# Kernel tuning notes

Hardware: AMD Instinct MI355X
Metric: run time of the kernel (lower is better)

## Reference

```python
import jax, jax.numpy as jnp
import numpy as np


def _maxpool2x2(x):
    # x: [N, C, H, W] -> [N, C, H//2, W//2]
    N, C, H, W = x.shape
    x = x.reshape(N, C, H // 2, 2, W // 2, 2)
    return x.max(axis=(3, 5))


def setup_inputs() -> dict:
    key = jax.random.key(0)
    ks = jax.random.split(key, 6)
    N, C, H, W = 16, 64, 64, 64
    x = jax.random.normal(ks[0], (N, C, H, W), dtype=jnp.float32)
    # 1x1 conv weights, stored as [out_ch, in_ch] (kernel is 1x1, no bias)
    w_theta = jax.random.normal(ks[1], (C >> 3, C), dtype=jnp.float32) * 0.05
    w_phi = jax.random.normal(ks[2], (C >> 3, C), dtype=jnp.float32) * 0.05
    w_g = jax.random.normal(ks[3], (C >> 1, C), dtype=jnp.float32) * 0.05
    w_o = jax.random.normal(ks[4], (C, C >> 1), dtype=jnp.float32) * 0.05
    gamma = jax.random.normal(ks[5], (), dtype=jnp.float32)
    return {"x": x, "w_theta": w_theta, "w_phi": w_phi, "w_g": w_g, "w_o": w_o, "gamma": gamma}


def reference(x, w_theta, w_phi, w_g, w_o, gamma):
    N, C, H, W = x.shape
    L = H * W           # location_num
    D = L >> 2          # downsampled_num
    # 1x1 convs as channel contractions
    theta = jnp.einsum('oc,nchw->nohw', w_theta, x).reshape(N, C >> 3, L)
    phi = _maxpool2x2(jnp.einsum('oc,nchw->nohw', w_phi, x)).reshape(N, C >> 3, D)
    attn = jax.nn.softmax(jnp.einsum('nkl,nkd->nld', theta, phi), axis=-1)  # [N, L, D]
    g = _maxpool2x2(jnp.einsum('oc,nchw->nohw', w_g, x)).reshape(N, C >> 1, D)
    attn_g = jnp.einsum('ngd,nld->ngl', g, attn).reshape(N, C >> 1, H, W)
    attn_g = jnp.einsum('og,nghw->nohw', w_o, attn_g)
    return x + gamma * attn_g
```

## Files before the change

kernel.cpp:

```cpp
#include <hip/hip_runtime.h>
#include <hip/hip_bf16.h>
#include <hip/hip_fp16.h>

#define NB 16
#define CCH 64
#define LL 4096
#define DD 1024

typedef _Float16 h8 __attribute__((ext_vector_type(8)));
typedef _Float16 h2 __attribute__((ext_vector_type(2)));
typedef float    f4v __attribute__((ext_vector_type(4)));

#if defined(__has_builtin)
#if __has_builtin(__builtin_amdgcn_fdot2)
#define HAVE_FDOT2 1
#endif
#if __has_builtin(__builtin_amdgcn_exp2f)
#define EXP2F(x) __builtin_amdgcn_exp2f(x)
#endif
#endif
#ifndef EXP2F
#define EXP2F(x) exp2f(x)
#endif

static __device__ __forceinline__ float fdot2f(h2 a, h2 b, float c) {
#ifdef HAVE_FDOT2
    return __builtin_amdgcn_fdot2(a, b, c, false);
#else
    return c + (float)a[0] * (float)b[0] + (float)a[1] * (float)b[1];
#endif
}

#define MFMA16(a, b, c) __builtin_amdgcn_mfma_f32_16x16x32_f16((a), (b), (c), 0, 0, 0)

__global__ __launch_bounds__(256) void prep_kernel(
    const float* __restrict__ x,
    const float* __restrict__ w_theta,
    const float* __restrict__ w_phi,
    const float* __restrict__ w_g,
    _Float16* __restrict__ theta_out,
    _Float16* __restrict__ phi_out,
    _Float16* __restrict__ gT_out)
{
    __shared__ float part[64][193];

    const int n    = blockIdx.x >> 6;
    const int rem  = blockIdx.x & 63;
    const int rg   = rem >> 1;
    const int half = rem & 1;
    const int tid  = threadIdx.x;
    const int cs   = tid >> 6;
    const int pix  = tid & 63;
    const int row  = pix >> 5;
    const int col  = pix & 31;
    const int l    = (rg * 2 + row) * 64 + half * 32 + col;

    const float* xp = x + (size_t)n * CCH * LL + l;
    float xv[16];
#pragma unroll
    for (int c = 0; c < 16; ++c) xv[c] = xp[(size_t)(cs * 16 + c) * LL];

    float f48[48];
#pragma unroll
    for (int k = 0; k < 8; ++k) {
        float a = 0.f;
        const float* w = w_theta + k * 64 + cs * 16;
#pragma unroll
        for (int c = 0; c < 16; ++c) a += w[c] * xv[c];
        f48[k] = a;
    }
#pragma unroll
    for (int k = 0; k < 8; ++k) {
        float a = 0.f;
        const float* w = w_phi + k * 64 + cs * 16;
#pragma unroll
        for (int c = 0; c < 16; ++c) a += w[c] * xv[c];
        f48[8 + k] = a;
    }
#pragma unroll
    for (int j = 0; j < 32; ++j) {
        float a = 0.f;
        const float* w = w_g + j * 64 + cs * 16;
#pragma unroll
        for (int c = 0; c < 16; ++c) a += w[c] * xv[c];
        f48[16 + j] = a;
    }

    {
        float* pp = &part[pix][cs * 48];
#pragma unroll
        for (int f = 0; f < 48; ++f) pp[f] = f48[f];
    }
    __syncthreads();

    float fin[12];
#pragma unroll
    for (int j = 0; j < 12; ++j) {
        int f = cs * 12 + j;
        fin[j] = part[pix][f] + part[pix][48 + f] + part[pix][96 + f] + part[pix][144 + f];
    }

    if (cs == 0) {
        h8 tv;
#pragma unroll
        for (int k = 0; k < 8; ++k) tv[k] = (_Float16)(fin[k] * 1.44269504f);
        *(h8*)(theta_out + ((size_t)n * LL + l) * 8) = tv;
    }

#pragma unroll
    for (int j = 0; j < 12; ++j) part[pix][cs * 12 + j] = fin[j];
    __syncthreads();

    for (int idx = tid; idx < 40 * 16; idx += 256) {
        int f8 = idx >> 4;
        int pc = idx & 15;
        int f  = 8 + f8;
        float v = fmaxf(fmaxf(part[2 * pc][f],      part[2 * pc + 1][f]),
                        fmaxf(part[32 + 2 * pc][f], part[33 + 2 * pc][f]));
        int d = rg * 32 + half * 16 + pc;
        if (f8 < 8) phi_out[((size_t)n * DD + d) * 8 + f8] = (_Float16)v;
        else        gT_out[((size_t)n * 32 + (f8 - 8)) * DD + d] = (_Float16)v;
    }
}

__global__ __launch_bounds__(256, 6) void attn_kernel(
    const float*    __restrict__ x,
    const _Float16* __restrict__ theta,
    const _Float16* __restrict__ phi,
    const _Float16* __restrict__ gT,
    const float*    __restrict__ w_o,
    const float*    __restrict__ gamma_p,
    float*          __restrict__ out)
{
    __shared__ __align__(16) char smem[18944 + 512];
    _Float16* phi_s  = (_Float16*)smem;
    float*    red    = (float*)smem;
    float*    out_s  = (float*)smem;
    float*    ssum_s = (float*)(smem + 18944);

    const int n    = blockIdx.x >> 7;
    const int lblk = blockIdx.x & 127;
    const int tid  = threadIdx.x;
    const int h    = tid >> 6;
    const int lane = tid & 63;
    const int m16  = lane & 15;
    const int quad = lane >> 4;
    const int l0   = lblk * 32;

    const _Float16* gT_n = gT + (size_t)n * 32 * DD;

    {
        const float4* ps = (const float4*)(phi + (size_t)n * DD * 8);
        float4* pd = (float4*)phi_s;
#pragma unroll
        for (int i = 0; i < 4; ++i) pd[tid + 256 * i] = ps[tid + 256 * i];
    }

    h8 th0 = *(const h8*)(theta + ((size_t)n * LL + l0 + m16) * 8);
    h8 th1 = *(const h8*)(theta + ((size_t)n * LL + l0 + 16 + m16) * 8);
    const h2* t0p = (const h2*)&th0;
    const h2* t1p = (const h2*)&th1;

    const int vp = h >> 1;
    h8 wof[2];
#pragma unroll
    for (int i = 0; i < 2; ++i) {
        const float* wr = w_o + (size_t)(m16 + 16 * (vp * 2 + i)) * 32 + quad * 8;
        float4 wa = *(const float4*)wr;
        float4 wb = *(const float4*)(wr + 4);
        wof[i][0] = (_Float16)wa.x; wof[i][1] = (_Float16)wa.y;
        wof[i][2] = (_Float16)wa.z; wof[i][3] = (_Float16)wa.w;
        wof[i][4] = (_Float16)wb.x; wof[i][5] = (_Float16)wb.y;
        wof[i][6] = (_Float16)wb.z; wof[i][7] = (_Float16)wb.w;
    }

    __syncthreads();

    f4v c00 = {0.f, 0.f, 0.f, 0.f}, c01 = c00, c10 = c00, c11 = c00;
    float ssum0 = 0.f, ssum1 = 0.f;

    const _Float16* gr0 = gT_n + (size_t)m16 * DD + h * 256 + quad * 8;
    const _Float16* gr1 = gT_n + (size_t)(16 + m16) * DD + h * 256 + quad * 8;
    const _Float16* pr  = phi_s + (size_t)(h * 256 + quad * 8) * 8;

#pragma unroll 2
    for (int c = 0; c < 8; ++c) {
        const int d0 = c * 32;
        h8 b0 = *(const h8*)(gr0 + d0);
        h8 b1 = *(const h8*)(gr1 + d0);
        h8 a0, a1;
#pragma unroll
        for (int j = 0; j < 8; ++j) {
            h8 ph = *(const h8*)(pr + (size_t)(d0 + j) * 8);
            const h2* pp = (const h2*)&ph;
            float s0 = fdot2f(t0p[0], pp[0], 0.f);
            s0 = fdot2f(t0p[1], pp[1], s0);
            s0 = fdot2f(t0p[2], pp[2], s0);
            s0 = fdot2f(t0p[3], pp[3], s0);
            float s1 = fdot2f(t1p[0], pp[0], 0.f);
            s1 = fdot2f(t1p[1], pp[1], s1);
            s1 = fdot2f(t1p[2], pp[2], s1);
            s1 = fdot2f(t1p[3], pp[3], s1);
            float e0 = EXP2F(s0);
            float e1 = EXP2F(s1);
            ssum0 += e0; ssum1 += e1;
            a0[j] = (_Float16)e0;
            a1[j] = (_Float16)e1;
        }
        c00 = MFMA16(a0, b0, c00);
        c01 = MFMA16(a0, b1, c01);
        c10 = MFMA16(a1, b0, c10);
        c11 = MFMA16(a1, b1, c11);
    }

    ssum0 += __shfl_xor(ssum0, 16); ssum0 += __shfl_xor(ssum0, 32);
    ssum1 += __shfl_xor(ssum1, 16); ssum1 += __shfl_xor(ssum1, 32);
    if (quad == 0) {
        ssum_s[h * 32 + m16]      = ssum0;
        ssum_s[h * 32 + 16 + m16] = ssum1;
    }
    __syncthreads();

    {
        float* rg = red + (size_t)h * 32 * 37;
#pragma unroll
        for (int r = 0; r < 4; ++r) {
            const int rr = quad * 4 + r;
            rg[rr * 37 + m16]             = c00[r];
            rg[rr * 37 + 16 + m16]        = c01[r];
            rg[(16 + rr) * 37 + m16]      = c10[r];
            rg[(16 + rr) * 37 + 16 + m16] = c11[r];
        }
    }
    __syncthreads();

    const int t = h & 1;
    h8 pa;
    {
        const int q = t * 16 + m16;
        const float* rq = red + q * 37 + quad * 8;
        float ss = ssum_s[q] + ssum_s[32 + q] + ssum_s[64 + q] + ssum_s[96 + q];
        float inv = 1.0f / ss;
#pragma unroll
        for (int j = 0; j < 8; ++j) {
            float sv = rq[j] + rq[32 * 37 + j] + rq[64 * 37 + j] + rq[96 * 37 + j];
            pa[j] = (_Float16)(sv * inv);
        }
    }
    __syncthreads();

    const f4v zero = {0.f, 0.f, 0.f, 0.f};
#pragma unroll
    for (int i = 0; i < 2; ++i) {
        f4v pv = MFMA16(pa, wof[i], zero);
        const int och = m16 + 16 * (vp * 2 + i);
        float* od = out_s + (size_t)(t * 16 + quad * 4) * 68 + och;
#pragma unroll
        for (int r = 0; r < 4; ++r) od[r * 68] = pv[r];
    }
    __syncthreads();

    const float gamma = gamma_p[0];
    const int soch = tid >> 2;
    const int qoff = (tid & 3) * 8;
    const float* xrow = x   + (size_t)n * CCH * LL + (size_t)soch * LL + l0 + qoff;
    float*       orow = out + (size_t)n * CCH * LL + (size_t)soch * LL + l0 + qoff;
#pragma unroll
    for (int i = 0; i < 2; ++i) {
        float4 xv = *(const float4*)(xrow + i * 4);
        float4 ov;
        ov.x = xv.x + gamma * out_s[(qoff + i * 4)     * 68 + soch];
        ov.y = xv.y + gamma * out_s[(qoff + i * 4 + 1) * 68 + soch];
        ov.z = xv.z + gamma * out_s[(qoff + i * 4 + 2) * 68 + soch];
        ov.w = xv.w + gamma * out_s[(qoff + i * 4 + 3) * 68 + soch];
        *(float4*)(orow + i * 4) = ov;
    }
}

extern "C" void kernel_launch(void* const* d_in, const int* in_sizes, int n_in,
                              void* d_out, int out_size, void* d_ws, size_t ws_size,
                              hipStream_t stream) {
    const float* x       = (const float*)d_in[0];
    const float* w_theta = (const float*)d_in[1];
    const float* w_phi   = (const float*)d_in[2];
    const float* w_g     = (const float*)d_in[3];
    const float* w_o     = (const float*)d_in[4];
    const float* gamma   = (const float*)d_in[5];
    float* out = (float*)d_out;

    _Float16* theta_h = (_Float16*)d_ws;
    _Float16* phi_h   = theta_h + (size_t)NB * LL * 8;
    _Float16* gT_h    = phi_h   + (size_t)NB * DD * 8;

    prep_kernel<<<1024, 256, 0, stream>>>(x, w_theta, w_phi, w_g,
                                          theta_h, phi_h, gT_h);
    attn_kernel<<<2048, 256, 0, stream>>>(x, theta_h, phi_h, gT_h,
                                          w_o, gamma, out);
}
```

Baseline: 131.5 us.

## Use fp16 prep scratch, pad phi LDS, split dot chains, raise occupancy

The prep kernel's shared reduction buffer moves from fp32 to fp16 packed pairs, which halves LDS use and allows a higher occupancy hint. The attention kernel pads the phi tile in LDS by one slot every eight entries to avoid bank conflicts. It splits each fdot2 dependency chain into two shorter chains and raises its launch-bounds occupancy from 6 to 8. Storing the partial channel sums in fp16 loses precision before the final sum and max-pool, and the tighter register budget may cause spills.

New measurement: 149.7 us. 1.14x slower.

```diff
diff --git a/kernel.cpp b/kernel.cpp
--- a/kernel.cpp
+++ b/kernel.cpp
@@ -33,7 +33,7 @@
 
 #define MFMA16(a, b, c) __builtin_amdgcn_mfma_f32_16x16x32_f16((a), (b), (c), 0, 0, 0)
 
-__global__ __launch_bounds__(256) void prep_kernel(
+__global__ __launch_bounds__(256, 6) void prep_kernel(
     const float* __restrict__ x,
     const float* __restrict__ w_theta,
     const float* __restrict__ w_phi,
@@ -42,7 +42,7 @@
     _Float16* __restrict__ phi_out,
     _Float16* __restrict__ gT_out)
 {
-    __shared__ float part[64][193];
+    __shared__ _Float16 part[64][198];
 
     const int n    = blockIdx.x >> 6;
     const int rem  = blockIdx.x & 63;
@@ -87,17 +87,26 @@
     }
 
     {
-        float* pp = &part[pix][cs * 48];
-#pragma unroll
-        for (int f = 0; f < 48; ++f) pp[f] = f48[f];
+        h2* pp = (h2*)&part[pix][cs * 48];
+#pragma unroll
+        for (int f2 = 0; f2 < 24; ++f2) {
+            h2 t;
+            t[0] = (_Float16)f48[2 * f2];
+            t[1] = (_Float16)f48[2 * f2 + 1];
+            pp[f2] = t;
+        }
     }
     __syncthreads();
 
     float fin[12];
-#pragma unroll
-    for (int j = 0; j < 12; ++j) {
-        int f = cs * 12 + j;
-        fin[j] = part[pix][f] + part[pix][48 + f] + part[pix][96 + f] + part[pix][144 + f];
+    {
+        const h2* rq = (const h2*)&part[pix][cs * 12];
+#pragma unroll
+        for (int jj = 0; jj < 6; ++jj) {
+            h2 a = rq[jj], b = rq[24 + jj], c = rq[48 + jj], d = rq[72 + jj];
+            fin[2 * jj]     = (float)a[0] + (float)b[0] + (float)c[0] + (float)d[0];
+            fin[2 * jj + 1] = (float)a[1] + (float)b[1] + (float)c[1] + (float)d[1];
+        }
     }
 
     if (cs == 0) {
@@ -107,23 +116,31 @@
         *(h8*)(theta_out + ((size_t)n * LL + l) * 8) = tv;
     }
 
-#pragma unroll
-    for (int j = 0; j < 12; ++j) part[pix][cs * 12 + j] = fin[j];
+    {
+        h2* wb = (h2*)&part[pix][cs * 12];
+#pragma unroll
+        for (int jj = 0; jj < 6; ++jj) {
+            h2 t;
+            t[0] = (_Float16)fin[2 * jj];
+            t[1] = (_Float16)fin[2 * jj + 1];
+            wb[jj] = t;
+        }
+    }
     __syncthreads();
 
     for (int idx = tid; idx < 40 * 16; idx += 256) {
         int f8 = idx >> 4;
         int pc = idx & 15;
         int f  = 8 + f8;
-        float v = fmaxf(fmaxf(part[2 * pc][f],      part[2 * pc + 1][f]),
-                        fmaxf(part[32 + 2 * pc][f], part[33 + 2 * pc][f]));
+        float v = fmaxf(fmaxf((float)part[2 * pc][f],      (float)part[2 * pc + 1][f]),
+                        fmaxf((float)part[32 + 2 * pc][f], (float)part[33 + 2 * pc][f]));
         int d = rg * 32 + half * 16 + pc;
         if (f8 < 8) phi_out[((size_t)n * DD + d) * 8 + f8] = (_Float16)v;
         else        gT_out[((size_t)n * 32 + (f8 - 8)) * DD + d] = (_Float16)v;
     }
 }
 
-__global__ __launch_bounds__(256, 6) void attn_kernel(
+__global__ __launch_bounds__(256, 8) void attn_kernel(
     const float*    __restrict__ x,
     const _Float16* __restrict__ theta,
     const _Float16* __restrict__ phi,
@@ -153,7 +170,10 @@
         const float4* ps = (const float4*)(phi + (size_t)n * DD * 8);
         float4* pd = (float4*)phi_s;
 #pragma unroll
-        for (int i = 0; i < 4; ++i) pd[tid + 256 * i] = ps[tid + 256 * i];
+        for (int i = 0; i < 4; ++i) {
+            const int d = tid + 256 * i;
+            pd[d + (d >> 3)] = ps[d];
+        }
     }
 
     h8 th0 = *(const h8*)(theta + ((size_t)n * LL + l0 + m16) * 8);
@@ -181,28 +201,30 @@
 
     const _Float16* gr0 = gT_n + (size_t)m16 * DD + h * 256 + quad * 8;
     const _Float16* gr1 = gT_n + (size_t)(16 + m16) * DD + h * 256 + quad * 8;
-    const _Float16* pr  = phi_s + (size_t)(h * 256 + quad * 8) * 8;
+    const int pb = h * 256 + quad * 8;
+    const _Float16* pr = phi_s + (size_t)(pb + (pb >> 3)) * 8;
 
 #pragma unroll 2
     for (int c = 0; c < 8; ++c) {
         const int d0 = c * 32;
         h8 b0 = *(const h8*)(gr0 + d0);
         h8 b1 = *(const h8*)(gr1 + d0);
+        const _Float16* prc = pr + c * 288;
         h8 a0, a1;
 #pragma unroll
         for (int j = 0; j < 8; ++j) {
-            h8 ph = *(const h8*)(pr + (size_t)(d0 + j) * 8);
+            h8 ph = *(const h8*)(prc + j * 8);
             const h2* pp = (const h2*)&ph;
-            float s0 = fdot2f(t0p[0], pp[0], 0.f);
-            s0 = fdot2f(t0p[1], pp[1], s0);
-            s0 = fdot2f(t0p[2], pp[2], s0);
-            s0 = fdot2f(t0p[3], pp[3], s0);
-            float s1 = fdot2f(t1p[0], pp[0], 0.f);
-            s1 = fdot2f(t1p[1], pp[1], s1);
-            s1 = fdot2f(t1p[2], pp[2], s1);
-            s1 = fdot2f(t1p[3], pp[3], s1);
-            float e0 = EXP2F(s0);
-            float e1 = EXP2F(s1);
+            float u0 = fdot2f(t0p[0], pp[0], 0.f);
+            u0 = fdot2f(t0p[1], pp[1], u0);
+            float v0 = fdot2f(t0p[2], pp[2], 0.f);
+            v0 = fdot2f(t0p[3], pp[3], v0);
+            float u1 = fdot2f(t1p[0], pp[0], 0.f);
+            u1 = fdot2f(t1p[1], pp[1], u1);
+            float v1 = fdot2f(t1p[2], pp[2], 0.f);
+            v1 = fdot2f(t1p[3], pp[3], v1);
+            float e0 = EXP2F(u0 + v0);
+            float e1 = EXP2F(u1 + v1);
             ssum0 += e0; ssum1 += e1;
             a0[j] = (_Float16)e0;
             a1[j] = (_Float16)e1;
```
